# Performance work log

Hardware: AMD Instinct MI355X
Metric: run time of the kernel (lower is better)

Reference implementation:

```python
import jax, jax.numpy as jnp
import numpy as np

D_MODEL = 512
NHEAD = 8
D_HEAD = D_MODEL // NHEAD
SCALE = D_HEAD ** -0.5
EPS = 1e-8


def setup_inputs() -> dict:
    key = jax.random.key(0)
    ks = jax.random.split(key, 12)
    B, N = 4, 2048
    s = D_MODEL ** -0.5
    return {
        "Q_input": jax.random.normal(ks[0], (B, N, D_MODEL), jnp.float32),
        "KV_input": jax.random.normal(ks[1], (B, N, D_MODEL), jnp.float32),
        "SC": jax.random.uniform(ks[2], (B, N, N), jnp.float32),
        "Wq_w": jax.random.normal(ks[3], (D_MODEL, D_MODEL), jnp.float32) * s,
        "Wq_b": jnp.zeros((D_MODEL,), jnp.float32),
        "Wk_w": jax.random.normal(ks[4], (D_MODEL, D_MODEL), jnp.float32) * s,
        "Wk_b": jnp.zeros((D_MODEL,), jnp.float32),
        "Wv_w": jax.random.normal(ks[5], (D_MODEL, D_MODEL), jnp.float32) * s,
        "Wv_b": jnp.zeros((D_MODEL,), jnp.float32),
        "gate_w": jax.random.normal(ks[6], (), jnp.float32),
        "gate_b": jnp.zeros((), jnp.float32),
        "out_w": jax.random.normal(ks[7], (D_MODEL, D_MODEL), jnp.float32) * s,
        "out_b": jnp.zeros((D_MODEL,), jnp.float32),
    }


def reference(Q_input, KV_input, SC, Wq_w, Wq_b, Wk_w, Wk_b, Wv_w, Wv_b,
              gate_w, gate_b, out_w, out_b):
    B, N, _ = Q_input.shape
    # projections -> [B, H, N, d_head]
    def proj(x, w, b):
        y = x @ w.T + b
        return y.reshape(B, N, NHEAD, D_HEAD).transpose(0, 2, 1, 3)
    Q = proj(Q_input, Wq_w, Wq_b)
    K = proj(KV_input, Wk_w, Wk_b)
    V = proj(KV_input, Wv_w, Wv_b)
    # scores [B, H, N, N]
    scores = jnp.einsum('bhqd,bhkd->bhqk', Q, K) * SCALE
    # per-edge gate: sigmoid(w*SC + b), broadcast over heads
    g = jax.nn.sigmoid(SC * gate_w + gate_b)  # [B, N, N]
    scores = scores + jnp.log(g + EPS)[:, None, :, :]
    attn = jax.nn.softmax(scores, axis=-1)
    out = jnp.einsum('bhqk,bhkd->bhqd', attn, V)
    out = out.transpose(0, 2, 1, 3).reshape(B, N, D_MODEL)
    return out @ out_w.T + out_b
```

## Files before the change

### kernel.cpp

```cpp
#include <hip/hip_runtime.h>

typedef unsigned short u16;
typedef unsigned int u32;
typedef __attribute__((ext_vector_type(4))) float f32x4;
typedef __attribute__((ext_vector_type(8))) short s16x8;
typedef __attribute__((ext_vector_type(4))) u16 u16x4;
typedef __attribute__((ext_vector_type(2))) u32 u32x2;

#define L2E 1.4426950408889634f
#define QSCALE 0.18033688011112042f

__device__ __forceinline__ u16 f2bf(float f) {
    union { float f; u32 i; } v; v.f = f;
    return (u16)((v.i + 0x7fffu + ((v.i >> 16) & 1u)) >> 16);
}
__device__ __forceinline__ u32 pack_hi(float a, float b) {
    union { float f; u32 i; } x, y; x.f = a; y.f = b;
    return (x.i >> 16) | (y.i & 0xFFFF0000u);
}
__device__ __forceinline__ float bflo(u32 w) {
    union { u32 i; float f; } v; v.i = w << 16; return v.f;
}
__device__ __forceinline__ float bfhi(u32 w) {
    union { u32 i; float f; } v; v.i = w & 0xFFFF0000u; return v.f;
}

__device__ __forceinline__ void gl2lds16(const u16* g, u16* l) {
    __builtin_amdgcn_global_load_lds(
        (const __attribute__((address_space(1))) void*)g,
        (__attribute__((address_space(3))) void*)l, 16, 0, 0);
}

__global__ __launch_bounds__(256) void prep_kernel(
    const float* __restrict__ s0, const float* __restrict__ s1,
    const float* __restrict__ s2, const float* __restrict__ s3,
    const float* __restrict__ s4, const float* __restrict__ s5,
    u16* __restrict__ dst,
    const float* __restrict__ SC, const float* __restrict__ gwp,
    const float* __restrict__ gbp, u16* __restrict__ LGx)
{
    if (blockIdx.x < 9216) {
        int e = (blockIdx.x * 256 + threadIdx.x) * 4;
        const float* src; int off;
        if      (e < 4194304) { src = s0; off = e; }
        else if (e < 8388608) { src = s1; off = e - 4194304; }
        else if (e < 8650752) { src = s2; off = e - 8388608; }
        else if (e < 8912896) { src = s3; off = e - 8650752; }
        else if (e < 9175040) { src = s4; off = e - 8912896; }
        else                  { src = s5; off = e - 9175040; }
        f32x4 f = *(const f32x4*)(src + off);
        u16x4 o;
#pragma unroll
        for (int j = 0; j < 4; ++j) o[j] = f2bf(f[j]);
        *(u16x4*)(dst + e) = o;
    } else {
        const int flat = (blockIdx.x - 9216) * 256 + threadIdx.x;
        const int lane = flat & 63;
        const int kt   = (flat >> 6) & 31;
        const int t16  = (flat >> 11) & 127;
        const int b    = flat >> 18;
        const int l16 = lane & 15, quad = lane >> 4;
        const float tA = -gwp[0] * L2E, tB = -gbp[0] * L2E;
        const float* row = SC + ((size_t)b * 2048 + t16 * 16 + l16) * 2048
                              + kt * 64 + quad * 4;
        __align__(16) u16 tmp[16];
#pragma unroll
        for (int kk = 0; kk < 4; ++kk) {
            f32x4 x = *(const f32x4*)(row + kk * 16);
#pragma unroll
            for (int reg = 0; reg < 4; ++reg) {
                float g = __builtin_amdgcn_rcpf(
                    1.0f + __builtin_amdgcn_exp2f(tA * x[reg] + tB)) + 1e-8f;
                tmp[kk * 4 + reg] = f2bf(__builtin_amdgcn_logf(g));
            }
        }
        u16* d = LGx + (size_t)flat * 16;
        *(uint4*)d       = *(uint4*)tmp;
        *(uint4*)(d + 8) = *(uint4*)(tmp + 8);
    }
}

__device__ __forceinline__ void gemm_core(
    const u16* __restrict__ A, const u16* __restrict__ Bw,
    int m0, int n0, u16* As, u16* Bs, f32x4 acc[4][4])
{
    const int tid = threadIdx.x;
    const int lane = tid & 63, w = tid >> 6;
    const int wm = w >> 1, wn = w & 1;
    const int l16 = lane & 15, quad = lane >> 4;
    const int srow = (lane >> 2), sch = (lane & 3) * 8;
    const f32x4 vzero = {0.f, 0.f, 0.f, 0.f};
#pragma unroll
    for (int i = 0; i < 4; ++i)
#pragma unroll
        for (int j = 0; j < 4; ++j) acc[i][j] = vzero;

#pragma unroll
    for (int j = 0; j < 2; ++j) {
        int row = w * 32 + j * 16 + srow;
        gl2lds16(&A[(size_t)(m0 + row) * 512 + sch], &As[w * 1024 + j * 512]);
        gl2lds16(&Bw[(size_t)(n0 + row) * 512 + sch], &Bs[w * 1024 + j * 512]);
    }
    for (int kt = 0; kt < 16; ++kt) {
        __syncthreads();
        const int cur = (kt & 1) * 4096;
        if (kt < 15) {
            const int nxt = ((kt + 1) & 1) * 4096;
#pragma unroll
            for (int j = 0; j < 2; ++j) {
                int row = w * 32 + j * 16 + srow;
                gl2lds16(&A[(size_t)(m0 + row) * 512 + (kt + 1) * 32 + sch],
                         &As[nxt + w * 1024 + j * 512]);
                gl2lds16(&Bw[(size_t)(n0 + row) * 512 + (kt + 1) * 32 + sch],
                         &Bs[nxt + w * 1024 + j * 512]);
            }
        }
        s16x8 af[4], bfr[4];
#pragma unroll
        for (int mt = 0; mt < 4; ++mt)
            af[mt] = *(const s16x8*)&As[cur + (wm * 64 + mt * 16 + l16) * 32 + quad * 8];
#pragma unroll
        for (int nt = 0; nt < 4; ++nt)
            bfr[nt] = *(const s16x8*)&Bs[cur + (wn * 64 + nt * 16 + l16) * 32 + quad * 8];
#pragma unroll
        for (int mt = 0; mt < 4; ++mt)
#pragma unroll
            for (int nt = 0; nt < 4; ++nt)
                acc[mt][nt] = __builtin_amdgcn_mfma_f32_16x16x32_bf16(
                    af[mt], bfr[nt], acc[mt][nt], 0, 0, 0);
    }
}

__global__ __launch_bounds__(256) void proj_kernel(
    const u16* __restrict__ cQin, const u16* __restrict__ cKV,
    const u16* __restrict__ cW,
    const float* __restrict__ bq, const float* __restrict__ bk,
    const float* __restrict__ bv,
    u16* __restrict__ Qh, u16* __restrict__ Kh, u16* __restrict__ Vt)
{
    __shared__ __align__(16) u16 As[2 * 4096];
    __shared__ __align__(16) u16 Bs[2 * 4096];
    const int job = blockIdx.z;
    const u16* A = (job == 0) ? cQin : cKV;
    const u16* W = cW + (size_t)job * 262144;
    const float* bias = (job == 0) ? bq : (job == 1 ? bk : bv);
    const int m0 = blockIdx.y * 128, n0 = blockIdx.x * 128;
    f32x4 acc[4][4];
    gemm_core(A, W, m0, n0, As, Bs, acc);

    const int tid = threadIdx.x, lane = tid & 63, w = tid >> 6;
    const int wm = w >> 1, wn = w & 1, l16 = lane & 15, quad = lane >> 4;
#pragma unroll
    for (int nt = 0; nt < 4; ++nt) {
        int j = n0 + wn * 64 + nt * 16 + l16;
        float bj = bias[j];
        int h = j >> 6, d = j & 63;
#pragma unroll
        for (int mt = 0; mt < 4; ++mt) {
            int trow = m0 + wm * 64 + mt * 16 + quad * 4;
            int bb = trow >> 11, nn = trow & 2047;
            int bh = bb * 8 + h;
            if (job == 2) {
                u16x4 pv;
#pragma unroll
                for (int reg = 0; reg < 4; ++reg) pv[reg] = f2bf(acc[mt][nt][reg] + bj);
                *(u16x4*)&Vt[(size_t)(bh * 64 + d) * 2048 + nn] = pv;
            } else if (job == 0) {
#pragma unroll
                for (int reg = 0; reg < 4; ++reg)
                    Qh[(size_t)(bh * 2048 + nn + reg) * 64 + d] =
                        f2bf((acc[mt][nt][reg] + bj) * QSCALE);
            } else {
#pragma unroll
                for (int reg = 0; reg < 4; ++reg)
                    Kh[(size_t)(bh * 2048 + nn + reg) * 64 + d] =
                        f2bf(acc[mt][nt][reg] + bj);
            }
        }
    }
}

__global__ __launch_bounds__(256, 2) void attn_kernel(
    const u16* __restrict__ Qh, const u16* __restrict__ Kh,
    const u16* __restrict__ Vt, const u16* __restrict__ LGx,
    u16* __restrict__ Ob)
{
    __shared__ __align__(16) u16 Ks[2][8192];
    __shared__ __align__(16) u16 Vs[2][8192];
    const int tid = threadIdx.x;
    const int w = tid >> 6, lane = tid & 63;
    const int l16 = lane & 15, quad = lane >> 4;
    const int b = blockIdx.z, head = blockIdx.y, qg = blockIdx.x;
    const int bh = b * 8 + head;
    const int q0a = qg * 128 + w * 32, q0b = q0a + 16;
    const int t16a = qg * 8 + w * 2;
    const u16* Qp = Qh + (size_t)bh * 131072;
    const u16* Kp = Kh + (size_t)bh * 131072;
    const u16* Vp = Vt + (size_t)bh * 131072;
    const u16* lgPa = LGx + ((size_t)((b * 128 + t16a) * 32) * 64 + lane) * 16;
    const u16* lgPb = LGx + ((size_t)((b * 128 + t16a + 1) * 32) * 64 + lane) * 16;
    const f32x4 vzero = {0.f, 0.f, 0.f, 0.f};
    const s16x8 ones = {0x3F80, 0x3F80, 0x3F80, 0x3F80,
                        0x3F80, 0x3F80, 0x3F80, 0x3F80};

    const int s3 = l16 & 7, s2x = s3 & 3, s4x = s3 & 4;
    const int qsw = (quad ^ s2x) * 8;
    const int rb0 = l16 * 64 + qsw + s4x * 8;
    const int rb1 = l16 * 64 + qsw + (4 ^ s4x) * 8;
    const u16* KbL = &Ks[0][0];
    const u16* VbL = &Vs[0][0];

    const int sr = lane >> 3, c8 = lane & 7;
    const bool isK = (w < 2);
    const int hv = w & 1;
    const u16* sgq = isK
        ? (Kp + (size_t)(hv * 64 + sr) * 64 + (c8 ^ sr) * 8)
        : (Vp + (size_t)sr * 2048 + hv * 64 + (c8 ^ sr) * 8);
    const size_t slabAdv = isK ? 512 : 16384;
    const size_t tileAdv = isK ? 8192 : 128;
    u16* sdb = isK ? &Ks[0][hv * 4096] : &Vs[0][hv * 4096];

    s16x8 qfa0 = *(const s16x8*)&Qp[(size_t)(q0a + l16) * 64 + quad * 8];
    s16x8 qfa1 = *(const s16x8*)&Qp[(size_t)(q0a + l16) * 64 + 32 + quad * 8];
    s16x8 qfb0 = *(const s16x8*)&Qp[(size_t)(q0b + l16) * 64 + quad * 8];
    s16x8 qfb1 = *(const s16x8*)&Qp[(size_t)(q0b + l16) * 64 + 32 + quad * 8];
    f32x4 oA[4], oB[4], laccA = vzero, laccB = vzero;
#pragma unroll
    for (int dn = 0; dn < 4; ++dn) { oA[dn] = vzero; oB[dn] = vzero; }

#pragma unroll
    for (int j = 0; j < 8; ++j)
        gl2lds16(sgq + (size_t)j * slabAdv, sdb + j * 512);
    sgq += tileAdv;
    uint4 lga0 = *(const uint4*)lgPa;
    uint4 lga1 = *(const uint4*)(lgPa + 8);
    uint4 lga2 = *(const uint4*)(lgPa + 1024);
    uint4 lga3 = *(const uint4*)(lgPa + 1032);
    uint4 lgb0 = *(const uint4*)lgPb;
    uint4 lgb1 = *(const uint4*)(lgPb + 8);
    uint4 lgb2 = *(const uint4*)(lgPb + 1024);
    uint4 lgb3 = *(const uint4*)(lgPb + 1032);
    lgPa += 2048; lgPb += 2048;

#define QKQUAD(LA, LB, MA, MB, KOFF)                                           \
    {                                                                          \
        const u32 wda[8] = {LA.x, LA.y, LA.z, LA.w, LB.x, LB.y, LB.z, LB.w};   \
        const u32 wdb[8] = {MA.x, MA.y, MA.z, MA.w, MB.x, MB.y, MB.z, MB.w};   \
        _Pragma("unroll")                                                      \
        for (int kk = 0; kk < 4; ++kk) {                                       \
            s16x8 ka = *(const s16x8*)(KbL + bo + rb0 + (KOFF + kk) * 1024);   \
            s16x8 kb = *(const s16x8*)(KbL + bo + rb1 + (KOFF + kk) * 1024);   \
            f32x4 ci;                                                          \
            ci[0] = bflo(wda[kk * 2]);     ci[1] = bfhi(wda[kk * 2]);          \
            ci[2] = bflo(wda[kk * 2 + 1]); ci[3] = bfhi(wda[kk * 2 + 1]);      \
            f32x4 s = __builtin_amdgcn_mfma_f32_16x16x32_bf16(ka, qfa0, ci, 0, 0, 0); \
            s = __builtin_amdgcn_mfma_f32_16x16x32_bf16(kb, qfa1, s, 0, 0, 0); \
            f32x4 cj;                                                          \
            cj[0] = bflo(wdb[kk * 2]);     cj[1] = bfhi(wdb[kk * 2]);          \
            cj[2] = bflo(wdb[kk * 2 + 1]); cj[3] = bfhi(wdb[kk * 2 + 1]);      \
            f32x4 t = __builtin_amdgcn_mfma_f32_16x16x32_bf16(ka, qfb0, cj, 0, 0, 0); \
            t = __builtin_amdgcn_mfma_f32_16x16x32_bf16(kb, qfb1, t, 0, 0, 0); \
            PwA[KOFF + kk][0] = pack_hi(__builtin_amdgcn_exp2f(s[0]),          \
                                        __builtin_amdgcn_exp2f(s[1]));         \
            PwA[KOFF + kk][1] = pack_hi(__builtin_amdgcn_exp2f(s[2]),          \
                                        __builtin_amdgcn_exp2f(s[3]));         \
            PwB[KOFF + kk][0] = pack_hi(__builtin_amdgcn_exp2f(t[0]),          \
                                        __builtin_amdgcn_exp2f(t[1]));         \
            PwB[KOFF + kk][1] = pack_hi(__builtin_amdgcn_exp2f(t[2]),          \
                                        __builtin_amdgcn_exp2f(t[3]));         \
        }                                                                      \
    }

    for (int kt = 0; kt < 16; ++kt) {
        __syncthreads();
        const int bo = (kt & 1) * 8192;
        if (kt < 15) {
            u16* dd = sdb + (8192 - bo);
#pragma unroll
            for (int j = 0; j < 8; ++j)
                gl2lds16(sgq + (size_t)j * slabAdv, dd + j * 512);
            sgq += tileAdv;
        }
        __builtin_amdgcn_s_setprio(1);
        u32 PwA[8][2], PwB[8][2];
        QKQUAD(lga0, lga1, lgb0, lgb1, 0);
        QKQUAD(lga2, lga3, lgb2, lgb3, 4);
        if (kt < 15) {
            lga0 = *(const uint4*)lgPa;
            lga1 = *(const uint4*)(lgPa + 8);
            lga2 = *(const uint4*)(lgPa + 1024);
            lga3 = *(const uint4*)(lgPa + 1032);
            lgb0 = *(const uint4*)lgPb;
            lgb1 = *(const uint4*)(lgPb + 8);
            lgb2 = *(const uint4*)(lgPb + 1024);
            lgb3 = *(const uint4*)(lgPb + 1032);
            lgPa += 2048; lgPb += 2048;
        }
#pragma unroll
        for (int kc = 0; kc < 4; ++kc) {
            union { u32 wrd[4]; s16x8 v; } pa, pb;
#pragma unroll
            for (int i = 0; i < 2; ++i) {
                u32x2 r1 = __builtin_amdgcn_permlane32_swap(
                    PwA[2 * kc][i], PwA[2 * kc + 1][i], false, false);
                u32x2 r2 = __builtin_amdgcn_permlane16_swap(
                    r1[0], r1[1], false, false);
                pa.wrd[i]     = r2[0];
                pa.wrd[2 + i] = r2[1];
                u32x2 r3 = __builtin_amdgcn_permlane32_swap(
                    PwB[2 * kc][i], PwB[2 * kc + 1][i], false, false);
                u32x2 r4 = __builtin_amdgcn_permlane16_swap(
                    r3[0], r3[1], false, false);
                pb.wrd[i]     = r4[0];
                pb.wrd[2 + i] = r4[1];
            }
            s16x8 pfa = pa.v, pfb = pb.v;
            laccA = __builtin_amdgcn_mfma_f32_16x16x32_bf16(pfa, ones, laccA, 0, 0, 0);
            laccB = __builtin_amdgcn_mfma_f32_16x16x32_bf16(pfb, ones, laccB, 0, 0, 0);
            const int vbb = ((kc & 1) ? rb1 : rb0) + (kc >> 1) * 4096 + bo;
#pragma unroll
            for (int dn = 0; dn < 4; ++dn) {
                s16x8 vf = *(const s16x8*)(VbL + vbb + dn * 1024);
                oA[dn] = __builtin_amdgcn_mfma_f32_16x16x32_bf16(
                    pfa, vf, oA[dn], 0, 0, 0);
                oB[dn] = __builtin_amdgcn_mfma_f32_16x16x32_bf16(
                    pfb, vf, oB[dn], 0, 0, 0);
            }
        }
        __builtin_amdgcn_s_setprio(0);
    }
#undef QKQUAD
#pragma unroll
    for (int reg = 0; reg < 4; ++reg) {
        float invA = __builtin_amdgcn_rcpf(laccA[reg]);
        float invB = __builtin_amdgcn_rcpf(laccB[reg]);
        int trowA = b * 2048 + q0a + quad * 4 + reg;
        int trowB = b * 2048 + q0b + quad * 4 + reg;
#pragma unroll
        for (int dn = 0; dn < 4; ++dn) {
            Ob[(size_t)trowA * 512 + head * 64 + dn * 16 + l16] =
                f2bf(oA[dn][reg] * invA);
            Ob[(size_t)trowB * 512 + head * 64 + dn * 16 + l16] =
                f2bf(oB[dn][reg] * invB);
        }
    }
}

__global__ __launch_bounds__(256) void out_kernel(
    const u16* __restrict__ Ob, const u16* __restrict__ cWo,
    const float* __restrict__ bo, float* __restrict__ out)
{
    __shared__ __align__(16) u16 As[2 * 4096];
    __shared__ __align__(16) u16 Bs[2 * 4096];
    const int m0 = blockIdx.y * 128, n0 = blockIdx.x * 128;
    f32x4 acc[4][4];
    gemm_core(Ob, cWo, m0, n0, As, Bs, acc);
    const int tid = threadIdx.x, lane = tid & 63, w = tid >> 6;
    const int wm = w >> 1, wn = w & 1, l16 = lane & 15, quad = lane >> 4;
#pragma unroll
    for (int nt = 0; nt < 4; ++nt) {
        int j = n0 + wn * 64 + nt * 16 + l16;
        float bj = bo[j];
#pragma unroll
        for (int mt = 0; mt < 4; ++mt) {
            int t = m0 + wm * 64 + mt * 16 + quad * 4;
#pragma unroll
            for (int reg = 0; reg < 4; ++reg)
                out[(size_t)(t + reg) * 512 + j] = acc[mt][nt][reg] + bj;
        }
    }
}

extern "C" void kernel_launch(void* const* d_in, const int* in_sizes, int n_in,
                              void* d_out, int out_size, void* d_ws, size_t ws_size,
                              hipStream_t stream)
{
    const float* Qin  = (const float*)d_in[0];
    const float* KVin = (const float*)d_in[1];
    const float* SC   = (const float*)d_in[2];
    const float* Wq   = (const float*)d_in[3];
    const float* bq   = (const float*)d_in[4];
    const float* Wk   = (const float*)d_in[5];
    const float* bk   = (const float*)d_in[6];
    const float* Wv   = (const float*)d_in[7];
    const float* bv   = (const float*)d_in[8];
    const float* gw   = (const float*)d_in[9];
    const float* gb   = (const float*)d_in[10];
    const float* Wo   = (const float*)d_in[11];
    const float* bo   = (const float*)d_in[12];
    float* out = (float*)d_out;

    u16* conv = (u16*)d_ws;
    u16* cQin = conv;
    u16* cKV  = conv + 4194304;
    u16* cW   = conv + 8388608;
    u16* Qh   = conv + 9437184;
    u16* Kh   = Qh + 4194304;
    u16* Vt   = Kh + 4194304;
    u16* Ob   = Vt + 4194304;
    u16* LGx  = Ob + 4194304;

    hipLaunchKernelGGL(prep_kernel, dim3(13312), dim3(256), 0, stream,
                       Qin, KVin, Wq, Wk, Wv, Wo, conv, SC, gw, gb, LGx);
    hipLaunchKernelGGL(proj_kernel, dim3(4, 64, 3), dim3(256), 0, stream,
                       cQin, cKV, cW, bq, bk, bv, Qh, Kh, Vt);
    hipLaunchKernelGGL(attn_kernel, dim3(16, 8, 4), dim3(256), 0, stream,
                       Qh, Kh, Vt, LGx, Ob);
    hipLaunchKernelGGL(out_kernel, dim3(4, 64), dim3(256), 0, stream,
                       Ob, cW + 786432, bo, out);
}
```

Before: 239.0 us.

## Software-pipeline attention QK and PV stages, shrink output GEMM tile rows

The attention loop is restructured so the QK^T/exp stage of tile k runs alongside the PV stage of tile k-1. K and V loads are staggered across separate LDS buffers, with P kept in two register sets. This is meant to overlap exp/permute work with MFMA and hide LDS latency, but it raises register pressure under launch bounds of 2 blocks. The output GEMM switches to 64-row tiles, doubling block count to improve CU fill, and pack_hi uses a single v_perm instruction.

```diff
diff --git a/kernel.cpp b/kernel.cpp
--- a/kernel.cpp
+++ b/kernel.cpp
@@ -16,7 +16,7 @@
 }
 __device__ __forceinline__ u32 pack_hi(float a, float b) {
     union { float f; u32 i; } x, y; x.f = a; y.f = b;
-    return (x.i >> 16) | (y.i & 0xFFFF0000u);
+    return __builtin_amdgcn_perm(y.i, x.i, 0x07060302u);
 }
 __device__ __forceinline__ float bflo(u32 w) {
     union { u32 i; float f; } v; v.i = w << 16; return v.f;
@@ -131,6 +131,57 @@
     }
 }
 
+__device__ __forceinline__ void gemm_core_m64(
+    const u16* __restrict__ A, const u16* __restrict__ Bw,
+    int m0, int n0, u16* As, u16* Bs, f32x4 acc[2][4])
+{
+    const int tid = threadIdx.x;
+    const int lane = tid & 63, w = tid >> 6;
+    const int wm = w & 1, wn = w >> 1;
+    const int l16 = lane & 15, quad = lane >> 4;
+    const int srow = (lane >> 2), sch = (lane & 3) * 8;
+    const f32x4 vzero = {0.f, 0.f, 0.f, 0.f};
+#pragma unroll
+    for (int i = 0; i < 2; ++i)
+#pragma unroll
+        for (int j = 0; j < 4; ++j) acc[i][j] = vzero;
+
+    gl2lds16(&A[(size_t)(m0 + w * 16 + srow) * 512 + sch], &As[w * 512]);
+#pragma unroll
+    for (int j = 0; j < 2; ++j) {
+        int row = w * 32 + j * 16 + srow;
+        gl2lds16(&Bw[(size_t)(n0 + row) * 512 + sch], &Bs[w * 1024 + j * 512]);
+    }
+    for (int kt = 0; kt < 16; ++kt) {
+        __syncthreads();
+        const int curA = (kt & 1) * 2048, curB = (kt & 1) * 4096;
+        if (kt < 15) {
+            const int nxtA = ((kt + 1) & 1) * 2048, nxtB = ((kt + 1) & 1) * 4096;
+            gl2lds16(&A[(size_t)(m0 + w * 16 + srow) * 512 + (kt + 1) * 32 + sch],
+                     &As[nxtA + w * 512]);
+#pragma unroll
+            for (int j = 0; j < 2; ++j) {
+                int row = w * 32 + j * 16 + srow;
+                gl2lds16(&Bw[(size_t)(n0 + row) * 512 + (kt + 1) * 32 + sch],
+                         &Bs[nxtB + w * 1024 + j * 512]);
+            }
+        }
+        s16x8 af[2], bfr[4];
+#pragma unroll
+        for (int mt = 0; mt < 2; ++mt)
+            af[mt] = *(const s16x8*)&As[curA + (wm * 32 + mt * 16 + l16) * 32 + quad * 8];
+#pragma unroll
+        for (int nt = 0; nt < 4; ++nt)
+            bfr[nt] = *(const s16x8*)&Bs[curB + (wn * 64 + nt * 16 + l16) * 32 + quad * 8];
+#pragma unroll
+        for (int mt = 0; mt < 2; ++mt)
+#pragma unroll
+            for (int nt = 0; nt < 4; ++nt)
+                acc[mt][nt] = __builtin_amdgcn_mfma_f32_16x16x32_bf16(
+                    af[mt], bfr[nt], acc[mt][nt], 0, 0, 0);
+    }
+}
+
 __global__ __launch_bounds__(256) void proj_kernel(
     const u16* __restrict__ cQin, const u16* __restrict__ cKV,
     const u16* __restrict__ cW,
@@ -185,8 +236,8 @@
     const u16* __restrict__ Vt, const u16* __restrict__ LGx,
     u16* __restrict__ Ob)
 {
-    __shared__ __align__(16) u16 Ks[2][8192];
-    __shared__ __align__(16) u16 Vs[2][8192];
+    __shared__ __align__(16) u16 Ks[2 * 8192];
+    __shared__ __align__(16) u16 Vs[2 * 8192];
     const int tid = threadIdx.x;
     const int w = tid >> 6, lane = tid & 63;
     const int l16 = lane & 15, quad = lane >> 4;
@@ -207,8 +258,8 @@
     const int qsw = (quad ^ s2x) * 8;
     const int rb0 = l16 * 64 + qsw + s4x * 8;
     const int rb1 = l16 * 64 + qsw + (4 ^ s4x) * 8;
-    const u16* KbL = &Ks[0][0];
-    const u16* VbL = &Vs[0][0];
+    u16* KsF = &Ks[0];
+    u16* VsF = &Vs[0];
 
     const int sr = lane >> 3, c8 = lane & 7;
     const bool isK = (w < 2);
@@ -218,7 +269,6 @@
         : (Vp + (size_t)sr * 2048 + hv * 64 + (c8 ^ sr) * 8);
     const size_t slabAdv = isK ? 512 : 16384;
     const size_t tileAdv = isK ? 8192 : 128;
-    u16* sdb = isK ? &Ks[0][hv * 4096] : &Vs[0][hv * 4096];
 
     s16x8 qfa0 = *(const s16x8*)&Qp[(size_t)(q0a + l16) * 64 + quad * 8];
     s16x8 qfa1 = *(const s16x8*)&Qp[(size_t)(q0a + l16) * 64 + 32 + quad * 8];
@@ -228,10 +278,13 @@
 #pragma unroll
     for (int dn = 0; dn < 4; ++dn) { oA[dn] = vzero; oB[dn] = vzero; }
 
-#pragma unroll
-    for (int j = 0; j < 8; ++j)
-        gl2lds16(sgq + (size_t)j * slabAdv, sdb + j * 512);
-    sgq += tileAdv;
+    if (isK) {
+        u16* db = KsF + hv * 4096;
+#pragma unroll
+        for (int j = 0; j < 8; ++j)
+            gl2lds16(sgq + (size_t)j * slabAdv, db + j * 512);
+        sgq += tileAdv;
+    }
     uint4 lga0 = *(const uint4*)lgPa;
     uint4 lga1 = *(const uint4*)(lgPa + 8);
     uint4 lga2 = *(const uint4*)(lgPa + 1024);
@@ -241,15 +294,16 @@
     uint4 lgb2 = *(const uint4*)(lgPb + 1024);
     uint4 lgb3 = *(const uint4*)(lgPb + 1032);
     lgPa += 2048; lgPb += 2048;
-
-#define QKQUAD(LA, LB, MA, MB, KOFF)                                           \
+    u32 PA0[8][2], PB0[8][2], PA1[8][2], PB1[8][2];
+
+#define QKPART(BO, PAp, PBp, LA, LB, MA, MB, KOFF)                             \
     {                                                                          \
         const u32 wda[8] = {LA.x, LA.y, LA.z, LA.w, LB.x, LB.y, LB.z, LB.w};   \
         const u32 wdb[8] = {MA.x, MA.y, MA.z, MA.w, MB.x, MB.y, MB.z, MB.w};   \
         _Pragma("unroll")                                                      \
         for (int kk = 0; kk < 4; ++kk) {                                       \
-            s16x8 ka = *(const s16x8*)(KbL + bo + rb0 + (KOFF + kk) * 1024);   \
-            s16x8 kb = *(const s16x8*)(KbL + bo + rb1 + (KOFF + kk) * 1024);   \
+            s16x8 ka = *(const s16x8*)(KsF + (BO) + rb0 + (KOFF + kk) * 1024); \
+            s16x8 kb = *(const s16x8*)(KsF + (BO) + rb1 + (KOFF + kk) * 1024); \
             f32x4 ci;                                                          \
             ci[0] = bflo(wda[kk * 2]);     ci[1] = bfhi(wda[kk * 2]);          \
             ci[2] = bflo(wda[kk * 2 + 1]); ci[3] = bfhi(wda[kk * 2 + 1]);      \
@@ -260,76 +314,90 @@
             cj[2] = bflo(wdb[kk * 2 + 1]); cj[3] = bfhi(wdb[kk * 2 + 1]);      \
             f32x4 t = __builtin_amdgcn_mfma_f32_16x16x32_bf16(ka, qfb0, cj, 0, 0, 0); \
             t = __builtin_amdgcn_mfma_f32_16x16x32_bf16(kb, qfb1, t, 0, 0, 0); \
-            PwA[KOFF + kk][0] = pack_hi(__builtin_amdgcn_exp2f(s[0]),          \
+            PAp[KOFF + kk][0] = pack_hi(__builtin_amdgcn_exp2f(s[0]),          \
                                         __builtin_amdgcn_exp2f(s[1]));         \
-            PwA[KOFF + kk][1] = pack_hi(__builtin_amdgcn_exp2f(s[2]),          \
+            PAp[KOFF + kk][1] = pack_hi(__builtin_amdgcn_exp2f(s[2]),          \
                                         __builtin_amdgcn_exp2f(s[3]));         \
-            PwB[KOFF + kk][0] = pack_hi(__builtin_amdgcn_exp2f(t[0]),          \
+            PBp[KOFF + kk][0] = pack_hi(__builtin_amdgcn_exp2f(t[0]),          \
                                         __builtin_amdgcn_exp2f(t[1]));         \
-            PwB[KOFF + kk][1] = pack_hi(__builtin_amdgcn_exp2f(t[2]),          \
+            PBp[KOFF + kk][1] = pack_hi(__builtin_amdgcn_exp2f(t[2]),          \
                                         __builtin_amdgcn_exp2f(t[3]));         \
         }                                                                      \
     }
 
-    for (int kt = 0; kt < 16; ++kt) {
-        __syncthreads();
-        const int bo = (kt & 1) * 8192;
-        if (kt < 15) {
-            u16* dd = sdb + (8192 - bo);
-#pragma unroll
-            for (int j = 0; j < 8; ++j)
-                gl2lds16(sgq + (size_t)j * slabAdv, dd + j * 512);
-            sgq += tileAdv;
-        }
-        __builtin_amdgcn_s_setprio(1);
-        u32 PwA[8][2], PwB[8][2];
-        QKQUAD(lga0, lga1, lgb0, lgb1, 0);
-        QKQUAD(lga2, lga3, lgb2, lgb3, 4);
-        if (kt < 15) {
-            lga0 = *(const uint4*)lgPa;
-            lga1 = *(const uint4*)(lgPa + 8);
-            lga2 = *(const uint4*)(lgPa + 1024);
-            lga3 = *(const uint4*)(lgPa + 1032);
-            lgb0 = *(const uint4*)lgPb;
-            lgb1 = *(const uint4*)(lgPb + 8);
-            lgb2 = *(const uint4*)(lgPb + 1024);
-            lgb3 = *(const uint4*)(lgPb + 1032);
-            lgPa += 2048; lgPb += 2048;
-        }
-#pragma unroll
-        for (int kc = 0; kc < 4; ++kc) {
-            union { u32 wrd[4]; s16x8 v; } pa, pb;
-#pragma unroll
-            for (int i = 0; i < 2; ++i) {
-                u32x2 r1 = __builtin_amdgcn_permlane32_swap(
-                    PwA[2 * kc][i], PwA[2 * kc + 1][i], false, false);
-                u32x2 r2 = __builtin_amdgcn_permlane16_swap(
-                    r1[0], r1[1], false, false);
-                pa.wrd[i]     = r2[0];
-                pa.wrd[2 + i] = r2[1];
-                u32x2 r3 = __builtin_amdgcn_permlane32_swap(
-                    PwB[2 * kc][i], PwB[2 * kc + 1][i], false, false);
-                u32x2 r4 = __builtin_amdgcn_permlane16_swap(
-                    r3[0], r3[1], false, false);
-                pb.wrd[i]     = r4[0];
-                pb.wrd[2 + i] = r4[1];
-            }
-            s16x8 pfa = pa.v, pfb = pb.v;
-            laccA = __builtin_amdgcn_mfma_f32_16x16x32_bf16(pfa, ones, laccA, 0, 0, 0);
-            laccB = __builtin_amdgcn_mfma_f32_16x16x32_bf16(pfb, ones, laccB, 0, 0, 0);
-            const int vbb = ((kc & 1) ? rb1 : rb0) + (kc >> 1) * 4096 + bo;
-#pragma unroll
-            for (int dn = 0; dn < 4; ++dn) {
-                s16x8 vf = *(const s16x8*)(VbL + vbb + dn * 1024);
-                oA[dn] = __builtin_amdgcn_mfma_f32_16x16x32_bf16(
-                    pfa, vf, oA[dn], 0, 0, 0);
-                oB[dn] = __builtin_amdgcn_mfma_f32_16x16x32_bf16(
-                    pfb, vf, oB[dn], 0, 0, 0);
-            }
-        }
-        __builtin_amdgcn_s_setprio(0);
-    }
-#undef QKQUAD
+#define PVPART(VRO, PAc, PBc)                                                  \
+    {                                                                          \
+        _Pragma("unroll")                                                      \
+        for (int kc = 0; kc < 4; ++kc) {                                       \
+            union { u32 wrd[4]; s16x8 v; } pa, pb;                             \
+            _Pragma("unroll")                                                  \
+            for (int i = 0; i < 2; ++i) {                                      \
+                u32x2 r1 = __builtin_amdgcn_permlane32_swap(                   \
+                    PAc[2 * kc][i], PAc[2 * kc + 1][i], false, false);         \
+                u32x2 r2 = __builtin_amdgcn_permlane16_swap(r1[0], r1[1], false, false); \
+                pa.wrd[i] = r2[0]; pa.wrd[2 + i] = r2[1];                      \
+                u32x2 r3 = __builtin_amdgcn_permlane32_swap(                   \
+                    PBc[2 * kc][i], PBc[2 * kc + 1][i], false, false);         \
+                u32x2 r4 = __builtin_amdgcn_permlane16_swap(r3[0], r3[1], false, false); \
+                pb.wrd[i] = r4[0]; pb.wrd[2 + i] = r4[1];                      \
+            }                                                                  \
+            s16x8 pfa = pa.v, pfb = pb.v;                                      \
+            laccA = __builtin_amdgcn_mfma_f32_16x16x32_bf16(pfa, ones, laccA, 0, 0, 0); \
+            laccB = __builtin_amdgcn_mfma_f32_16x16x32_bf16(pfb, ones, laccB, 0, 0, 0); \
+            const int vbb = ((kc & 1) ? rb1 : rb0) + (kc >> 1) * 4096 + (VRO); \
+            _Pragma("unroll")                                                  \
+            for (int dn = 0; dn < 4; ++dn) {                                   \
+                s16x8 vf = *(const s16x8*)(VsF + vbb + dn * 1024);             \
+                oA[dn] = __builtin_amdgcn_mfma_f32_16x16x32_bf16(pfa, vf, oA[dn], 0, 0, 0); \
+                oB[dn] = __builtin_amdgcn_mfma_f32_16x16x32_bf16(pfb, vf, oB[dn], 0, 0, 0); \
+            }                                                                  \
+        }                                                                      \
+    }
+
+#define AB(BO, PAp, PBp, PAc, PBc, DOPV, DOKST, DOLG)                          \
+    {                                                                          \
+        if (isK) {                                                             \
+            if (DOKST) {                                                       \
+                u16* db = KsF + (8192 - (BO)) + hv * 4096;                     \
+                _Pragma("unroll")                                              \
+                for (int j = 0; j < 8; ++j)                                    \
+                    gl2lds16(sgq + (size_t)j * 512, db + j * 512);             \
+                sgq += 8192;                                                   \
+            }                                                                  \
+        } else {                                                               \
+            u16* db = VsF + (BO) + hv * 4096;                                  \
+            _Pragma("unroll")                                                  \
+            for (int j = 0; j < 8; ++j)                                        \
+                gl2lds16(sgq + (size_t)j * 16384, db + j * 512);               \
+            sgq += 128;                                                        \
+        }                                                                      \
+        __builtin_amdgcn_s_setprio(1);                                         \
+        QKPART(BO, PAp, PBp, lga0, lga1, lgb0, lgb1, 0);                       \
+        QKPART(BO, PAp, PBp, lga2, lga3, lgb2, lgb3, 4);                       \
+        if (DOLG) {                                                            \
+            lga0 = *(const uint4*)lgPa; lga1 = *(const uint4*)(lgPa + 8);      \
+            lga2 = *(const uint4*)(lgPa + 1024); lga3 = *(const uint4*)(lgPa + 1032); \
+            lgb0 = *(const uint4*)lgPb; lgb1 = *(const uint4*)(lgPb + 8);      \
+            lgb2 = *(const uint4*)(lgPb + 1024); lgb3 = *(const uint4*)(lgPb + 1032); \
+            lgPa += 2048; lgPb += 2048;                                        \
+        }                                                                      \
+        if (DOPV) { PVPART((8192 - (BO)), PAc, PBc); }                         \
+        __builtin_amdgcn_s_setprio(0);                                         \
+        __syncthreads();                                                       \
+    }
+
+    __syncthreads();
+    AB(0,    PA0, PB0, PA1, PB1, false, true, true)
+    AB(8192, PA1, PB1, PA0, PB0, true,  true, true)
+    for (int kt2 = 2; kt2 < 16; kt2 += 2) {
+        AB(0,    PA0, PB0, PA1, PB1, true, true, true)
+        AB(8192, PA1, PB1, PA0, PB0, true, (kt2 < 14), (kt2 < 14))
+    }
+    PVPART(8192, PA1, PB1)
+#undef AB
+#undef QKPART
+#undef PVPART
+
 #pragma unroll
     for (int reg = 0; reg < 4; ++reg) {
         float invA = __builtin_amdgcn_rcpf(laccA[reg]);
@@ -350,20 +418,20 @@
     const u16* __restrict__ Ob, const u16* __restrict__ cWo,
     const float* __restrict__ bo, float* __restrict__ out)
 {
-    __shared__ __align__(16) u16 As[2 * 4096];
+    __shared__ __align__(16) u16 As[2 * 2048];
     __shared__ __align__(16) u16 Bs[2 * 4096];
-    const int m0 = blockIdx.y * 128, n0 = blockIdx.x * 128;
-    f32x4 acc[4][4];
-    gemm_core(Ob, cWo, m0, n0, As, Bs, acc);
+    const int m0 = blockIdx.y * 64, n0 = blockIdx.x * 128;
+    f32x4 acc[2][4];
+    gemm_core_m64(Ob, cWo, m0, n0, As, Bs, acc);
     const int tid = threadIdx.x, lane = tid & 63, w = tid >> 6;
-    const int wm = w >> 1, wn = w & 1, l16 = lane & 15, quad = lane >> 4;
+    const int wm = w & 1, wn = w >> 1, l16 = lane & 15, quad = lane >> 4;
 #pragma unroll
     for (int nt = 0; nt < 4; ++nt) {
         int j = n0 + wn * 64 + nt * 16 + l16;
         float bj = bo[j];
 #pragma unroll
-        for (int mt = 0; mt < 4; ++mt) {
-            int t = m0 + wm * 64 + mt * 16 + quad * 4;
+        for (int mt = 0; mt < 2; ++mt) {
+            int t = m0 + wm * 32 + mt * 16 + quad * 4;
 #pragma unroll
             for (int reg = 0; reg < 4; ++reg)
                 out[(size_t)(t + reg) * 512 + j] = acc[mt][nt][reg] + bj;
@@ -406,6 +474,6 @@
                        cQin, cKV, cW, bq, bk, bv, Qh, Kh, Vt);
     hipLaunchKernelGGL(attn_kernel, dim3(16, 8, 4), dim3(256), 0, stream,
                        Qh, Kh, Vt, LGx, Ob);
-    hipLaunchKernelGGL(out_kernel, dim3(4, 64), dim3(256), 0, stream,
+    hipLaunchKernelGGL(out_kernel, dim3(4, 128), dim3(256), 0, stream,
                        Ob, cW + 786432, bo, out);
 }
```

After: 243.3 us. No clear change (+1.8%).

## Co-schedule QKV projection with gate log precompute, halve output GEMM M-tile

Applied to the files above, without the earlier changes.

The SC gate-log precompute moves out of the conversion kernel and into the projection kernel, so the memory-bound gate pass (reading the 64MB SC tensor) shares a launch with the compute-bound QKV GEMMs and the two can overlap on the GPU. The output projection now uses a 64-row M tile, doubling its block count to fill more CUs. pack_hi becomes a single v_perm byte-permute, and the attention QK macro's second half is expanded inline with explicit pointer aliasing. The gate blocks share the projection kernel's LDS allocation, which may reduce occupancy for those blocks.

```diff
diff --git a/kernel.cpp b/kernel.cpp
--- a/kernel.cpp
+++ b/kernel.cpp
@@ -16,7 +16,7 @@
 }
 __device__ __forceinline__ u32 pack_hi(float a, float b) {
     union { float f; u32 i; } x, y; x.f = a; y.f = b;
-    return (x.i >> 16) | (y.i & 0xFFFF0000u);
+    return __builtin_amdgcn_perm(y.i, x.i, 0x07060302u);
 }
 __device__ __forceinline__ float bflo(u32 w) {
     union { u32 i; float f; } v; v.i = w << 16; return v.f;
@@ -31,30 +31,182 @@
         (__attribute__((address_space(3))) void*)l, 16, 0, 0);
 }
 
-__global__ __launch_bounds__(256) void prep_kernel(
+__global__ __launch_bounds__(256) void conv_kernel(
     const float* __restrict__ s0, const float* __restrict__ s1,
     const float* __restrict__ s2, const float* __restrict__ s3,
     const float* __restrict__ s4, const float* __restrict__ s5,
-    u16* __restrict__ dst,
+    u16* __restrict__ dst)
+{
+    int e = (blockIdx.x * 256 + threadIdx.x) * 4;
+    const float* src; int off;
+    if      (e < 4194304) { src = s0; off = e; }
+    else if (e < 8388608) { src = s1; off = e - 4194304; }
+    else if (e < 8650752) { src = s2; off = e - 8388608; }
+    else if (e < 8912896) { src = s3; off = e - 8650752; }
+    else if (e < 9175040) { src = s4; off = e - 8912896; }
+    else                  { src = s5; off = e - 9175040; }
+    f32x4 f = *(const f32x4*)(src + off);
+    u16x4 o;
+#pragma unroll
+    for (int j = 0; j < 4; ++j) o[j] = f2bf(f[j]);
+    *(u16x4*)(dst + e) = o;
+}
+
+__device__ __forceinline__ void gemm_core(
+    const u16* __restrict__ A, const u16* __restrict__ Bw,
+    int m0, int n0, u16* As, u16* Bs, f32x4 acc[4][4])
+{
+    const int tid = threadIdx.x;
+    const int lane = tid & 63, w = tid >> 6;
+    const int wm = w >> 1, wn = w & 1;
+    const int l16 = lane & 15, quad = lane >> 4;
+    const int srow = (lane >> 2), sch = (lane & 3) * 8;
+    const f32x4 vzero = {0.f, 0.f, 0.f, 0.f};
+#pragma unroll
+    for (int i = 0; i < 4; ++i)
+#pragma unroll
+        for (int j = 0; j < 4; ++j) acc[i][j] = vzero;
+
+#pragma unroll
+    for (int j = 0; j < 2; ++j) {
+        int row = w * 32 + j * 16 + srow;
+        gl2lds16(&A[(size_t)(m0 + row) * 512 + sch], &As[w * 1024 + j * 512]);
+        gl2lds16(&Bw[(size_t)(n0 + row) * 512 + sch], &Bs[w * 1024 + j * 512]);
+    }
+    for (int kt = 0; kt < 16; ++kt) {
+        __syncthreads();
+        const int cur = (kt & 1) * 4096;
+        if (kt < 15) {
+            const int nxt = ((kt + 1) & 1) * 4096;
+#pragma unroll
+            for (int j = 0; j < 2; ++j) {
+                int row = w * 32 + j * 16 + srow;
+                gl2lds16(&A[(size_t)(m0 + row) * 512 + (kt + 1) * 32 + sch],
+                         &As[nxt + w * 1024 + j * 512]);
+                gl2lds16(&Bw[(size_t)(n0 + row) * 512 + (kt + 1) * 32 + sch],
+                         &Bs[nxt + w * 1024 + j * 512]);
+            }
+        }
+        s16x8 af[4], bfr[4];
+#pragma unroll
+        for (int mt = 0; mt < 4; ++mt)
+            af[mt] = *(const s16x8*)&As[cur + (wm * 64 + mt * 16 + l16) * 32 + quad * 8];
+#pragma unroll
+        for (int nt = 0; nt < 4; ++nt)
+            bfr[nt] = *(const s16x8*)&Bs[cur + (wn * 64 + nt * 16 + l16) * 32 + quad * 8];
+#pragma unroll
+        for (int mt = 0; mt < 4; ++mt)
+#pragma unroll
+            for (int nt = 0; nt < 4; ++nt)
+                acc[mt][nt] = __builtin_amdgcn_mfma_f32_16x16x32_bf16(
+                    af[mt], bfr[nt], acc[mt][nt], 0, 0, 0);
+    }
+}
+
+__device__ __forceinline__ void gemm_core_m64(
+    const u16* __restrict__ A, const u16* __restrict__ Bw,
+    int m0, int n0, u16* As, u16* Bs, f32x4 acc[2][4])
+{
+    const int tid = threadIdx.x;
+    const int lane = tid & 63, w = tid >> 6;
+    const int wm = w & 1, wn = w >> 1;
+    const int l16 = lane & 15, quad = lane >> 4;
+    const int srow = (lane >> 2), sch = (lane & 3) * 8;
+    const f32x4 vzero = {0.f, 0.f, 0.f, 0.f};
+#pragma unroll
+    for (int i = 0; i < 2; ++i)
+#pragma unroll
+        for (int j = 0; j < 4; ++j) acc[i][j] = vzero;
+
+    gl2lds16(&A[(size_t)(m0 + w * 16 + srow) * 512 + sch], &As[w * 512]);
+#pragma unroll
+    for (int j = 0; j < 2; ++j) {
+        int row = w * 32 + j * 16 + srow;
+        gl2lds16(&Bw[(size_t)(n0 + row) * 512 + sch], &Bs[w * 1024 + j * 512]);
+    }
+    for (int kt = 0; kt < 16; ++kt) {
+        __syncthreads();
+        const int curA = (kt & 1) * 2048, curB = (kt & 1) * 4096;
+        if (kt < 15) {
+            const int nxtA = ((kt + 1) & 1) * 2048, nxtB = ((kt + 1) & 1) * 4096;
+            gl2lds16(&A[(size_t)(m0 + w * 16 + srow) * 512 + (kt + 1) * 32 + sch],
+                     &As[nxtA + w * 512]);
+#pragma unroll
+            for (int j = 0; j < 2; ++j) {
+                int row = w * 32 + j * 16 + srow;
+                gl2lds16(&Bw[(size_t)(n0 + row) * 512 + (kt + 1) * 32 + sch],
+                         &Bs[nxtB + w * 1024 + j * 512]);
+            }
+        }
+        s16x8 af[2], bfr[4];
+#pragma unroll
+        for (int mt = 0; mt < 2; ++mt)
+            af[mt] = *(const s16x8*)&As[curA + (wm * 32 + mt * 16 + l16) * 32 + quad * 8];
+#pragma unroll
+        for (int nt = 0; nt < 4; ++nt)
+            bfr[nt] = *(const s16x8*)&Bs[curB + (wn * 64 + nt * 16 + l16) * 32 + quad * 8];
+#pragma unroll
+        for (int mt = 0; mt < 2; ++mt)
+#pragma unroll
+            for (int nt = 0; nt < 4; ++nt)
+                acc[mt][nt] = __builtin_amdgcn_mfma_f32_16x16x32_bf16(
+                    af[mt], bfr[nt], acc[mt][nt], 0, 0, 0);
+    }
+}
+
+__global__ __launch_bounds__(256) void projlg_kernel(
+    const u16* __restrict__ cQin, const u16* __restrict__ cKV,
+    const u16* __restrict__ cW,
+    const float* __restrict__ bq, const float* __restrict__ bk,
+    const float* __restrict__ bv,
+    u16* __restrict__ Qh, u16* __restrict__ Kh, u16* __restrict__ Vt,
     const float* __restrict__ SC, const float* __restrict__ gwp,
     const float* __restrict__ gbp, u16* __restrict__ LGx)
 {
-    if (blockIdx.x < 9216) {
-        int e = (blockIdx.x * 256 + threadIdx.x) * 4;
-        const float* src; int off;
-        if      (e < 4194304) { src = s0; off = e; }
-        else if (e < 8388608) { src = s1; off = e - 4194304; }
-        else if (e < 8650752) { src = s2; off = e - 8388608; }
-        else if (e < 8912896) { src = s3; off = e - 8650752; }
-        else if (e < 9175040) { src = s4; off = e - 8912896; }
-        else                  { src = s5; off = e - 9175040; }
-        f32x4 f = *(const f32x4*)(src + off);
-        u16x4 o;
-#pragma unroll
-        for (int j = 0; j < 4; ++j) o[j] = f2bf(f[j]);
-        *(u16x4*)(dst + e) = o;
+    __shared__ __align__(16) u16 As[2 * 4096];
+    __shared__ __align__(16) u16 Bs[2 * 4096];
+    if (blockIdx.x < 768) {
+        const int job = blockIdx.x >> 8;
+        const int rem = blockIdx.x & 255;
+        const int n0 = (rem & 3) * 128, m0 = (rem >> 2) * 128;
+        const u16* A = (job == 0) ? cQin : cKV;
+        const u16* W = cW + (size_t)job * 262144;
+        const float* bias = (job == 0) ? bq : (job == 1 ? bk : bv);
+        f32x4 acc[4][4];
+        gemm_core(A, W, m0, n0, As, Bs, acc);
+
+        const int tid = threadIdx.x, lane = tid & 63, w = tid >> 6;
+        const int wm = w >> 1, wn = w & 1, l16 = lane & 15, quad = lane >> 4;
+#pragma unroll
+        for (int nt = 0; nt < 4; ++nt) {
+            int j = n0 + wn * 64 + nt * 16 + l16;
+            float bj = bias[j];
+            int h = j >> 6, d = j & 63;
+#pragma unroll
+            for (int mt = 0; mt < 4; ++mt) {
+                int trow = m0 + wm * 64 + mt * 16 + quad * 4;
+                int bb = trow >> 11, nn = trow & 2047;
+                int bh = bb * 8 + h;
+                if (job == 2) {
+                    u16x4 pv;
+#pragma unroll
+                    for (int reg = 0; reg < 4; ++reg) pv[reg] = f2bf(acc[mt][nt][reg] + bj);
+                    *(u16x4*)&Vt[(size_t)(bh * 64 + d) * 2048 + nn] = pv;
+                } else if (job == 0) {
+#pragma unroll
+                    for (int reg = 0; reg < 4; ++reg)
+                        Qh[(size_t)(bh * 2048 + nn + reg) * 64 + d] =
+                            f2bf((acc[mt][nt][reg] + bj) * QSCALE);
+                } else {
+#pragma unroll
+                    for (int reg = 0; reg < 4; ++reg)
+                        Kh[(size_t)(bh * 2048 + nn + reg) * 64 + d] =
+                            f2bf(acc[mt][nt][reg] + bj);
+                }
+            }
+        }
     } else {
-        const int flat = (blockIdx.x - 9216) * 256 + threadIdx.x;
+        const int flat = (blockIdx.x - 768) * 256 + threadIdx.x;
         const int lane = flat & 63;
         const int kt   = (flat >> 6) & 31;
         const int t16  = (flat >> 11) & 127;
@@ -77,106 +229,6 @@
         u16* d = LGx + (size_t)flat * 16;
         *(uint4*)d       = *(uint4*)tmp;
         *(uint4*)(d + 8) = *(uint4*)(tmp + 8);
-    }
-}
-
-__device__ __forceinline__ void gemm_core(
-    const u16* __restrict__ A, const u16* __restrict__ Bw,
-    int m0, int n0, u16* As, u16* Bs, f32x4 acc[4][4])
-{
-    const int tid = threadIdx.x;
-    const int lane = tid & 63, w = tid >> 6;
-    const int wm = w >> 1, wn = w & 1;
-    const int l16 = lane & 15, quad = lane >> 4;
-    const int srow = (lane >> 2), sch = (lane & 3) * 8;
-    const f32x4 vzero = {0.f, 0.f, 0.f, 0.f};
-#pragma unroll
-    for (int i = 0; i < 4; ++i)
-#pragma unroll
-        for (int j = 0; j < 4; ++j) acc[i][j] = vzero;
-
-#pragma unroll
-    for (int j = 0; j < 2; ++j) {
-        int row = w * 32 + j * 16 + srow;
-        gl2lds16(&A[(size_t)(m0 + row) * 512 + sch], &As[w * 1024 + j * 512]);
-        gl2lds16(&Bw[(size_t)(n0 + row) * 512 + sch], &Bs[w * 1024 + j * 512]);
-    }
-    for (int kt = 0; kt < 16; ++kt) {
-        __syncthreads();
-        const int cur = (kt & 1) * 4096;
-        if (kt < 15) {
-            const int nxt = ((kt + 1) & 1) * 4096;
-#pragma unroll
-            for (int j = 0; j < 2; ++j) {
-                int row = w * 32 + j * 16 + srow;
-                gl2lds16(&A[(size_t)(m0 + row) * 512 + (kt + 1) * 32 + sch],
-                         &As[nxt + w * 1024 + j * 512]);
-                gl2lds16(&Bw[(size_t)(n0 + row) * 512 + (kt + 1) * 32 + sch],
-                         &Bs[nxt + w * 1024 + j * 512]);
-            }
-        }
-        s16x8 af[4], bfr[4];
-#pragma unroll
-        for (int mt = 0; mt < 4; ++mt)
-            af[mt] = *(const s16x8*)&As[cur + (wm * 64 + mt * 16 + l16) * 32 + quad * 8];
-#pragma unroll
-        for (int nt = 0; nt < 4; ++nt)
-            bfr[nt] = *(const s16x8*)&Bs[cur + (wn * 64 + nt * 16 + l16) * 32 + quad * 8];
-#pragma unroll
-        for (int mt = 0; mt < 4; ++mt)
-#pragma unroll
-            for (int nt = 0; nt < 4; ++nt)
-                acc[mt][nt] = __builtin_amdgcn_mfma_f32_16x16x32_bf16(
-                    af[mt], bfr[nt], acc[mt][nt], 0, 0, 0);
-    }
-}
-
-__global__ __launch_bounds__(256) void proj_kernel(
-    const u16* __restrict__ cQin, const u16* __restrict__ cKV,
-    const u16* __restrict__ cW,
-    const float* __restrict__ bq, const float* __restrict__ bk,
-    const float* __restrict__ bv,
-    u16* __restrict__ Qh, u16* __restrict__ Kh, u16* __restrict__ Vt)
-{
-    __shared__ __align__(16) u16 As[2 * 4096];
-    __shared__ __align__(16) u16 Bs[2 * 4096];
-    const int job = blockIdx.z;
-    const u16* A = (job == 0) ? cQin : cKV;
-    const u16* W = cW + (size_t)job * 262144;
-    const float* bias = (job == 0) ? bq : (job == 1 ? bk : bv);
-    const int m0 = blockIdx.y * 128, n0 = blockIdx.x * 128;
-    f32x4 acc[4][4];
-    gemm_core(A, W, m0, n0, As, Bs, acc);
-
-    const int tid = threadIdx.x, lane = tid & 63, w = tid >> 6;
-    const int wm = w >> 1, wn = w & 1, l16 = lane & 15, quad = lane >> 4;
-#pragma unroll
-    for (int nt = 0; nt < 4; ++nt) {
-        int j = n0 + wn * 64 + nt * 16 + l16;
-        float bj = bias[j];
-        int h = j >> 6, d = j & 63;
-#pragma unroll
-        for (int mt = 0; mt < 4; ++mt) {
-            int trow = m0 + wm * 64 + mt * 16 + quad * 4;
-            int bb = trow >> 11, nn = trow & 2047;
-            int bh = bb * 8 + h;
-            if (job == 2) {
-                u16x4 pv;
-#pragma unroll
-                for (int reg = 0; reg < 4; ++reg) pv[reg] = f2bf(acc[mt][nt][reg] + bj);
-                *(u16x4*)&Vt[(size_t)(bh * 64 + d) * 2048 + nn] = pv;
-            } else if (job == 0) {
-#pragma unroll
-                for (int reg = 0; reg < 4; ++reg)
-                    Qh[(size_t)(bh * 2048 + nn + reg) * 64 + d] =
-                        f2bf((acc[mt][nt][reg] + bj) * QSCALE);
-            } else {
-#pragma unroll
-                for (int reg = 0; reg < 4; ++reg)
-                    Kh[(size_t)(bh * 2048 + nn + reg) * 64 + d] =
-                        f2bf(acc[mt][nt][reg] + bj);
-            }
-        }
     }
 }
 
@@ -248,8 +300,8 @@
         const u32 wdb[8] = {MA.x, MA.y, MA.z, MA.w, MB.x, MB.y, MB.z, MB.w};   \
         _Pragma("unroll")                                                      \
         for (int kk = 0; kk < 4; ++kk) {                                       \
-            s16x8 ka = *(const s16x8*)(KbL + bo + rb0 + (KOFF + kk) * 1024);   \
-            s16x8 kb = *(const s16x8*)(KbL + bo + rb1 + (KOFF + kk) * 1024);   \
+            s16x8 ka = *(const s16x8*)(KbL + bo + rb0 + kk * 1024);            \
+            s16x8 kb = *(const s16x8*)(KbL + bo + rb1 + kk * 1024);            \
             f32x4 ci;                                                          \
             ci[0] = bflo(wda[kk * 2]);     ci[1] = bfhi(wda[kk * 2]);          \
             ci[2] = bflo(wda[kk * 2 + 1]); ci[3] = bfhi(wda[kk * 2 + 1]);      \
@@ -260,14 +312,14 @@
             cj[2] = bflo(wdb[kk * 2 + 1]); cj[3] = bfhi(wdb[kk * 2 + 1]);      \
             f32x4 t = __builtin_amdgcn_mfma_f32_16x16x32_bf16(ka, qfb0, cj, 0, 0, 0); \
             t = __builtin_amdgcn_mfma_f32_16x16x32_bf16(kb, qfb1, t, 0, 0, 0); \
-            PwA[KOFF + kk][0] = pack_hi(__builtin_amdgcn_exp2f(s[0]),          \
-                                        __builtin_amdgcn_exp2f(s[1]));         \
-            PwA[KOFF + kk][1] = pack_hi(__builtin_amdgcn_exp2f(s[2]),          \
-                                        __builtin_amdgcn_exp2f(s[3]));         \
-            PwB[KOFF + kk][0] = pack_hi(__builtin_amdgcn_exp2f(t[0]),          \
-                                        __builtin_amdgcn_exp2f(t[1]));         \
-            PwB[KOFF + kk][1] = pack_hi(__builtin_amdgcn_exp2f(t[2]),          \
-                                        __builtin_amdgcn_exp2f(t[3]));         \
+            PwA[kk][0] = pack_hi(__builtin_amdgcn_exp2f(s[0]),                 \
+                                 __builtin_amdgcn_exp2f(s[1]));                \
+            PwA[kk][1] = pack_hi(__builtin_amdgcn_exp2f(s[2]),                 \
+                                 __builtin_amdgcn_exp2f(s[3]));                \
+            PwB[kk][0] = pack_hi(__builtin_amdgcn_exp2f(t[0]),                 \
+                                 __builtin_amdgcn_exp2f(t[1]));                \
+            PwB[kk][1] = pack_hi(__builtin_amdgcn_exp2f(t[2]),                 \
+                                 __builtin_amdgcn_exp2f(t[3]));                \
         }                                                                      \
     }
 
@@ -282,9 +334,47 @@
             sgq += tileAdv;
         }
         __builtin_amdgcn_s_setprio(1);
-        u32 PwA[8][2], PwB[8][2];
-        QKQUAD(lga0, lga1, lgb0, lgb1, 0);
-        QKQUAD(lga2, lga3, lgb2, lgb3, 4);
+        u32 PwA8[8][2], PwB8[8][2];
+        {
+            u32 (*PwA)[2] = &PwA8[0];
+            u32 (*PwB)[2] = &PwB8[0];
+            QKQUAD(lga0, lga1, lgb0, lgb1, 0);
+        }
+        {
+            const int bo2 = bo + 4096;
+            u32 (*PwA)[2] = &PwA8[4];
+            u32 (*PwB)[2] = &PwB8[4];
+            const int bo_save = bo2 - 4096;
+            {
+                const u32 wda[8] = {lga2.x, lga2.y, lga2.z, lga2.w,
+                                    lga3.x, lga3.y, lga3.z, lga3.w};
+                const u32 wdb[8] = {lgb2.x, lgb2.y, lgb2.z, lgb2.w,
+                                    lgb3.x, lgb3.y, lgb3.z, lgb3.w};
+#pragma unroll
+                for (int kk = 0; kk < 4; ++kk) {
+                    s16x8 ka = *(const s16x8*)(KbL + bo_save + rb0 + (4 + kk) * 1024);
+                    s16x8 kb = *(const s16x8*)(KbL + bo_save + rb1 + (4 + kk) * 1024);
+                    f32x4 ci;
+                    ci[0] = bflo(wda[kk * 2]);     ci[1] = bfhi(wda[kk * 2]);
+                    ci[2] = bflo(wda[kk * 2 + 1]); ci[3] = bfhi(wda[kk * 2 + 1]);
+                    f32x4 s = __builtin_amdgcn_mfma_f32_16x16x32_bf16(ka, qfa0, ci, 0, 0, 0);
+                    s = __builtin_amdgcn_mfma_f32_16x16x32_bf16(kb, qfa1, s, 0, 0, 0);
+                    f32x4 cj;
+                    cj[0] = bflo(wdb[kk * 2]);     cj[1] = bfhi(wdb[kk * 2]);
+                    cj[2] = bflo(wdb[kk * 2 + 1]); cj[3] = bfhi(wdb[kk * 2 + 1]);
+                    f32x4 t = __builtin_amdgcn_mfma_f32_16x16x32_bf16(ka, qfb0, cj, 0, 0, 0);
+                    t = __builtin_amdgcn_mfma_f32_16x16x32_bf16(kb, qfb1, t, 0, 0, 0);
+                    PwA[kk][0] = pack_hi(__builtin_amdgcn_exp2f(s[0]),
+                                         __builtin_amdgcn_exp2f(s[1]));
+                    PwA[kk][1] = pack_hi(__builtin_amdgcn_exp2f(s[2]),
+                                         __builtin_amdgcn_exp2f(s[3]));
+                    PwB[kk][0] = pack_hi(__builtin_amdgcn_exp2f(t[0]),
+                                         __builtin_amdgcn_exp2f(t[1]));
+                    PwB[kk][1] = pack_hi(__builtin_amdgcn_exp2f(t[2]),
+                                         __builtin_amdgcn_exp2f(t[3]));
+                }
+            }
+        }
         if (kt < 15) {
             lga0 = *(const uint4*)lgPa;
             lga1 = *(const uint4*)(lgPa + 8);
@@ -302,13 +392,13 @@
 #pragma unroll
             for (int i = 0; i < 2; ++i) {
                 u32x2 r1 = __builtin_amdgcn_permlane32_swap(
-                    PwA[2 * kc][i], PwA[2 * kc + 1][i], false, false);
+                    PwA8[2 * kc][i], PwA8[2 * kc + 1][i], false, false);
                 u32x2 r2 = __builtin_amdgcn_permlane16_swap(
                     r1[0], r1[1], false, false);
                 pa.wrd[i]     = r2[0];
                 pa.wrd[2 + i] = r2[1];
                 u32x2 r3 = __builtin_amdgcn_permlane32_swap(
-                    PwB[2 * kc][i], PwB[2 * kc + 1][i], false, false);
+                    PwB8[2 * kc][i], PwB8[2 * kc + 1][i], false, false);
                 u32x2 r4 = __builtin_amdgcn_permlane16_swap(
                     r3[0], r3[1], false, false);
                 pb.wrd[i]     = r4[0];
@@ -350,20 +440,20 @@
     const u16* __restrict__ Ob, const u16* __restrict__ cWo,
     const float* __restrict__ bo, float* __restrict__ out)
 {
-    __shared__ __align__(16) u16 As[2 * 4096];
+    __shared__ __align__(16) u16 As[2 * 2048];
     __shared__ __align__(16) u16 Bs[2 * 4096];
-    const int m0 = blockIdx.y * 128, n0 = blockIdx.x * 128;
-    f32x4 acc[4][4];
-    gemm_core(Ob, cWo, m0, n0, As, Bs, acc);
+    const int m0 = blockIdx.y * 64, n0 = blockIdx.x * 128;
+    f32x4 acc[2][4];
+    gemm_core_m64(Ob, cWo, m0, n0, As, Bs, acc);
     const int tid = threadIdx.x, lane = tid & 63, w = tid >> 6;
-    const int wm = w >> 1, wn = w & 1, l16 = lane & 15, quad = lane >> 4;
+    const int wm = w & 1, wn = w >> 1, l16 = lane & 15, quad = lane >> 4;
 #pragma unroll
     for (int nt = 0; nt < 4; ++nt) {
         int j = n0 + wn * 64 + nt * 16 + l16;
         float bj = bo[j];
 #pragma unroll
-        for (int mt = 0; mt < 4; ++mt) {
-            int t = m0 + wm * 64 + mt * 16 + quad * 4;
+        for (int mt = 0; mt < 2; ++mt) {
+            int t = m0 + wm * 32 + mt * 16 + quad * 4;
 #pragma unroll
             for (int reg = 0; reg < 4; ++reg)
                 out[(size_t)(t + reg) * 512 + j] = acc[mt][nt][reg] + bj;
@@ -400,12 +490,13 @@
     u16* Ob   = Vt + 4194304;
     u16* LGx  = Ob + 4194304;
 
-    hipLaunchKernelGGL(prep_kernel, dim3(13312), dim3(256), 0, stream,
-                       Qin, KVin, Wq, Wk, Wv, Wo, conv, SC, gw, gb, LGx);
-    hipLaunchKernelGGL(proj_kernel, dim3(4, 64, 3), dim3(256), 0, stream,
-                       cQin, cKV, cW, bq, bk, bv, Qh, Kh, Vt);
+    hipLaunchKernelGGL(conv_kernel, dim3(9216), dim3(256), 0, stream,
+                       Qin, KVin, Wq, Wk, Wv, Wo, conv);
+    hipLaunchKernelGGL(projlg_kernel, dim3(4864), dim3(256), 0, stream,
+                       cQin, cKV, cW, bq, bk, bv, Qh, Kh, Vt,
+                       SC, gw, gb, LGx);
     hipLaunchKernelGGL(attn_kernel, dim3(16, 8, 4), dim3(256), 0, stream,
                        Qh, Kh, Vt, LGx, Ob);
-    hipLaunchKernelGGL(out_kernel, dim3(4, 64), dim3(256), 0, stream,
+    hipLaunchKernelGGL(out_kernel, dim3(4, 128), dim3(256), 0, stream,
                        Ob, cW + 786432, bo, out);
 }
```

After: 235.9 us. No clear change (-1.3%).
